# Kernel optimization log

Hardware: AMD Instinct MI355X
Metric: run time of the kernel (lower is better)

## Reference

```python
import jax, jax.numpy as jnp
import numpy as np


def setup_inputs() -> dict:
    key = jax.random.key(0)
    k1, k2 = jax.random.split(key)
    surfaces = jax.random.normal(k1, (4, 4096, 3), dtype=jnp.float32)   # [S, N, K]
    targets = jax.random.normal(k2, (16384, 3), dtype=jnp.float32)      # [M, K]
    return {"surfaces": surfaces, "targets": targets}


def reference(surfaces, targets):
    # Pairwise squared distances ||a-b||^2 = ||a||^2 + ||b||^2 - 2 a.b
    # surfaces: [S, N, K], targets: [M, K]
    a2 = jnp.sum(surfaces * surfaces, axis=-1)          # [S, N]
    b2 = jnp.sum(targets * targets, axis=-1)            # [M]
    ab = jnp.einsum('snk,mk->snm', surfaces, targets)   # [S, N, M]
    dist = a2[:, :, None] + b2[None, None, :] - 2.0 * ab  # [S, N, M]
    # direction='cloud2nearest' -> dim=0: min over surface points N per target
    nearest = jnp.min(dist, axis=1)                     # [S, M]
    # stack over surfaces then min over dim 0 (S)
    nearest = jnp.min(nearest, axis=0)                  # [M]
    return jnp.sum(nearest)
```

## Files before the change

kernel.cpp:

```cpp
#include <hip/hip_runtime.h>
#include <cfloat>


namespace {
constexpr int M   = 16384;
constexpr int SN  = 16384;
constexpr int TPB = 256;
constexpr int T   = 8;
constexpr int TGT_PER_BLOCK = TPB * T;
constexpr int NCHUNK = 64;
constexpr int CHUNK  = SN / NCHUNK;
}

__global__ __launch_bounds__(TPB) void dist_partial_min(
    const float* __restrict__ surf,
    const float* __restrict__ tgt,
    float* __restrict__ wmin)
{
  __shared__ alignas(16) float4 spt[CHUNK];

  const int tid   = threadIdx.x;
  const int mbase = blockIdx.x * TGT_PER_BLOCK;
  const int cbase = blockIdx.y * CHUNK;

  {
    const float* s = surf + (size_t)(cbase + tid) * 3;
    const float x = s[0], y = s[1], z = s[2];
    spt[tid] = make_float4(x, y, z, fmaf(x, x, fmaf(y, y, z * z)));
  }

  float tx[T], ty[T], tz[T], b2[T], mn[T];
#pragma unroll
  for (int j = 0; j < T; ++j) {
    const int m     = mbase + j * TPB + tid;
    const float* tp = tgt + (size_t)m * 3;
    const float a = tp[0], b = tp[1], c = tp[2];
    tx[j] = -2.0f * a; ty[j] = -2.0f * b; tz[j] = -2.0f * c;
    b2[j] = fmaf(a, a, fmaf(b, b, c * c));
    mn[j] = FLT_MAX;
  }
  __syncthreads();

  for (int p = 0; p < CHUNK; p += 4) {
    const float4 P0 = spt[p + 0];
    const float4 P1 = spt[p + 1];
    const float4 P2 = spt[p + 2];
    const float4 P3 = spt[p + 3];
#pragma unroll
    for (int j = 0; j < T; ++j) {
      const float d0 = fmaf(P0.x, tx[j], fmaf(P0.y, ty[j], fmaf(P0.z, tz[j], P0.w)));
      const float d1 = fmaf(P1.x, tx[j], fmaf(P1.y, ty[j], fmaf(P1.z, tz[j], P1.w)));
      const float d2 = fmaf(P2.x, tx[j], fmaf(P2.y, ty[j], fmaf(P2.z, tz[j], P2.w)));
      const float d3 = fmaf(P3.x, tx[j], fmaf(P3.y, ty[j], fmaf(P3.z, tz[j], P3.w)));
      mn[j] = fminf(fminf(mn[j], d0), d1);
      mn[j] = fminf(fminf(mn[j], d2), d3);
    }
  }

#pragma unroll
  for (int j = 0; j < T; ++j)
    wmin[(size_t)blockIdx.y * M + mbase + j * TPB + tid] = mn[j] + b2[j];
}

__global__ __launch_bounds__(256) void dist_min_sum(
    const float* __restrict__ wmin,
    float* __restrict__ part)
{
  const int tid = threadIdx.x;
  const int m   = blockIdx.x * 256 + tid;

  float mnv = FLT_MAX;
  for (int c = 0; c < NCHUNK; ++c)
    mnv = fminf(mnv, wmin[(size_t)c * M + m]);

  float sum = mnv;
  for (int off = 32; off; off >>= 1) sum += __shfl_down(sum, off, 64);

  __shared__ float red[4];
  if ((tid & 63) == 0) red[tid >> 6] = sum;
  __syncthreads();
  if (tid == 0) part[blockIdx.x] = red[0] + red[1] + red[2] + red[3];
}

__global__ __launch_bounds__(64) void dist_final(
    const float* __restrict__ part, float* __restrict__ out)
{
  float v = part[threadIdx.x];
  for (int off = 32; off; off >>= 1) v += __shfl_down(v, off, 64);
  if (threadIdx.x == 0) out[0] = v;
}

extern "C" void kernel_launch(void* const* d_in, const int* in_sizes, int n_in,
                              void* d_out, int out_size, void* d_ws, size_t ws_size,
                              hipStream_t stream) {
  const float* surf = (const float*)d_in[0];
  const float* tgt  = (const float*)d_in[1];
  float* out  = (float*)d_out;
  float* wmin = (float*)d_ws;
  float* part = wmin + (size_t)NCHUNK * M;

  dim3 g1(M / TGT_PER_BLOCK, NCHUNK);
  dist_partial_min<<<g1, TPB, 0, stream>>>(surf, tgt, wmin);
  dist_min_sum<<<M / 256, 256, 0, stream>>>(wmin, part);
  dist_final<<<1, 64, 0, stream>>>(part, out);
}
```

Baseline: 39.20 us.

## Retile distance kernel, split over more chunks, fuse final reduction via atomic counter

Doubles targets per thread (T=16) and splits surface points into 256 chunks of 64, so the grid becomes 4x256 blocks each handling fewer points. The final reduce kernel is removed: the min-sum kernel now uses 64-thread blocks, and the last block to finish, detected with an atomic counter, sums the partials. This saves a kernel launch but makes the intermediate buffer four times larger (256x16384 floats) and the reduction reads 256 chunks per target, which may cost more memory traffic. The counter is reset from inside the first kernel.

Result: slower. 75.45 us (+92.5%).

```diff
diff --git a/kernel.cpp b/kernel.cpp
--- a/kernel.cpp
+++ b/kernel.cpp
@@ -6,16 +6,18 @@
 constexpr int M   = 16384;
 constexpr int SN  = 16384;
 constexpr int TPB = 256;
-constexpr int T   = 8;
+constexpr int T   = 16;
 constexpr int TGT_PER_BLOCK = TPB * T;
-constexpr int NCHUNK = 64;
+constexpr int NCHUNK = 256;
 constexpr int CHUNK  = SN / NCHUNK;
+constexpr int K2B = 256;
 }
 
-__global__ __launch_bounds__(TPB) void dist_partial_min(
+__global__ __launch_bounds__(TPB, 4) void dist_partial_min(
     const float* __restrict__ surf,
     const float* __restrict__ tgt,
-    float* __restrict__ wmin)
+    float* __restrict__ wmin,
+    unsigned* __restrict__ counter)
 {
   __shared__ alignas(16) float4 spt[CHUNK];
 
@@ -23,7 +25,9 @@
   const int mbase = blockIdx.x * TGT_PER_BLOCK;
   const int cbase = blockIdx.y * CHUNK;
 
-  {
+  if (blockIdx.x == 0 && blockIdx.y == 0 && tid == 0) counter[0] = 0u;
+
+  if (tid < CHUNK) {
     const float* s = surf + (size_t)(cbase + tid) * 3;
     const float x = s[0], y = s[1], z = s[2];
     spt[tid] = make_float4(x, y, z, fmaf(x, x, fmaf(y, y, z * z)));
@@ -62,12 +66,14 @@
     wmin[(size_t)blockIdx.y * M + mbase + j * TPB + tid] = mn[j] + b2[j];
 }
 
-__global__ __launch_bounds__(256) void dist_min_sum(
+__global__ __launch_bounds__(64) void dist_min_sum(
     const float* __restrict__ wmin,
-    float* __restrict__ part)
+    float* __restrict__ part,
+    unsigned* __restrict__ counter,
+    float* __restrict__ out)
 {
   const int tid = threadIdx.x;
-  const int m   = blockIdx.x * 256 + tid;
+  const int m   = blockIdx.x * 64 + tid;
 
   float mnv = FLT_MAX;
   for (int c = 0; c < NCHUNK; ++c)
@@ -76,18 +82,22 @@
   float sum = mnv;
   for (int off = 32; off; off >>= 1) sum += __shfl_down(sum, off, 64);
 
-  __shared__ float red[4];
-  if ((tid & 63) == 0) red[tid >> 6] = sum;
-  __syncthreads();
-  if (tid == 0) part[blockIdx.x] = red[0] + red[1] + red[2] + red[3];
-}
+  unsigned done = 0;
+  if (tid == 0) {
+    part[blockIdx.x] = sum;
+    __threadfence();
+    done = atomicAdd(counter, 1u);
+  }
+  done = __shfl(done, 0, 64);
 
-__global__ __launch_bounds__(64) void dist_final(
-    const float* __restrict__ part, float* __restrict__ out)
-{
-  float v = part[threadIdx.x];
-  for (int off = 32; off; off >>= 1) v += __shfl_down(v, off, 64);
-  if (threadIdx.x == 0) out[0] = v;
+  if (done == (unsigned)(K2B - 1)) {
+    __threadfence();
+    float v = 0.0f;
+#pragma unroll
+    for (int i = 0; i < K2B / 64; ++i) v += part[i * 64 + tid];
+    for (int off = 32; off; off >>= 1) v += __shfl_down(v, off, 64);
+    if (tid == 0) out[0] = v;
+  }
 }
 
 extern "C" void kernel_launch(void* const* d_in, const int* in_sizes, int n_in,
@@ -95,12 +105,13 @@
                               hipStream_t stream) {
   const float* surf = (const float*)d_in[0];
   const float* tgt  = (const float*)d_in[1];
-  float* out  = (float*)d_out;
-  float* wmin = (float*)d_ws;
-  float* part = wmin + (size_t)NCHUNK * M;
+  float* out = (float*)d_out;
+
+  float*    wmin    = (float*)d_ws;
+  float*    part    = wmin + (size_t)NCHUNK * M;
+  unsigned* counter = (unsigned*)(part + K2B);
 
   dim3 g1(M / TGT_PER_BLOCK, NCHUNK);
-  dist_partial_min<<<g1, TPB, 0, stream>>>(surf, tgt, wmin);
-  dist_min_sum<<<M / 256, 256, 0, stream>>>(wmin, part);
-  dist_final<<<1, 64, 0, stream>>>(part, out);
+  dist_partial_min<<<g1, TPB, 0, stream>>>(surf, tgt, wmin, counter);
+  dist_min_sum<<<K2B, 64, 0, stream>>>(wmin, part, counter, out);
 }
```
